# Kernel optimization log

Hardware: AMD Instinct MI355X
Metric: run time of the kernel (lower is better)

The kernel has to match this reference:

```python
import jax, jax.numpy as jnp
import numpy as np

SIZE = 512
N_STROKES = 8
N_SAMPLES = 32
STROKE_WIDTH = 0.04


def setup_inputs() -> dict:
    key = jax.random.key(0)
    k1, _ = jax.random.split(key)
    # control points seeded like torch.rand(...) * 0.6 + 0.2
    control_points = jax.random.uniform(k1, (N_STROKES, 4, 2), dtype=jnp.float32) * 0.6 + 0.2
    # pixel grid buffer: (x, y) coords in [0,1], row-major over (y, x)
    coords = jnp.linspace(0.0, 1.0, SIZE, dtype=jnp.float32)
    grid_y, grid_x = jnp.meshgrid(coords, coords, indexing="ij")
    pixel_grid = jnp.stack([grid_x, grid_y], axis=-1).reshape(-1, 2)  # (HW, 2)
    return {"control_points": control_points, "pixel_grid": pixel_grid}


def _bezier3_samples(curves, n_samples):
    # curves: (S, 4, 2) -> (S, n_samples, 2)
    ts = jnp.linspace(0.0, 1.0, n_samples, dtype=curves.dtype)
    t = ts[None, :, None]
    mt = 1.0 - t
    p0, p1, p2, p3 = (curves[:, k:k + 1, :] for k in range(4))
    return mt ** 3 * p0 + 3.0 * mt ** 2 * t * p1 + 3.0 * mt * t ** 2 * p2 + t ** 3 * p3


def reference(control_points, pixel_grid):
    # all_strokes(): symmetric=False, empty stroke_groups -> just clamp
    pts = jnp.clip(control_points, 0.0, 1.0)
    samples = _bezier3_samples(pts, N_SAMPLES).reshape(-1, 2)  # (P, 2), P = S*n_samples
    sharpness = float(N_SAMPLES) * 8.0
    # pairwise distances (HW, P) — soft-min via logsumexp over curve points
    diff = pixel_grid[:, None, :] - samples[None, :, :]          # (HW, P, 2)
    dist = jnp.sqrt(jnp.sum(diff * diff, axis=-1))               # (HW, P)
    min_dist = -jax.nn.logsumexp(-sharpness * dist, axis=-1) / sharpness  # (HW,)
    coverage = jax.nn.sigmoid((STROKE_WIDTH - min_dist) * (8.0 / STROKE_WIDTH))
    return (1.0 - coverage.reshape(SIZE, SIZE))[None]  # (1, H, W)
```

## Files before the change

kernel.cpp:

```cpp
#include <hip/hip_runtime.h>


#define SIZE 512
#define RADIUS 0.06f
#define FARCUT 0.1217f
#define HB 0.01467710f
#define HD 0.02075670f

__device__ __forceinline__ float clamp01(float x) {
    return fminf(fmaxf(x, 0.0f), 1.0f);
}
__device__ __forceinline__ float wave_min(float v) {
    #pragma unroll
    for (int m = 1; m < 64; m <<= 1) v = fminf(v, __shfl_xor(v, m));
    return v;
}
__device__ __forceinline__ float wave_max(float v) {
    #pragma unroll
    for (int m = 1; m < 64; m <<= 1) v = fmaxf(v, __shfl_xor(v, m));
    return v;
}

__global__ __launch_bounds__(256) void bezier_glyph_kernel(
        const float* __restrict__ cp,
        float* __restrict__ out)
{
    __shared__ float2 list1[260];
    __shared__ float2 list2[260];
    __shared__ float  redbuf[8];
    __shared__ int    n1s, n2s;

    const int tid  = threadIdx.x;
    const int lane = tid & 63;
    const int wid  = tid >> 6;
    if (tid == 0) { n1s = 0; n2s = 0; }

    const int b        = blockIdx.x;
    const int row_base = (b >> 5) << 4;
    const int col_base = (b & 31) << 4;
    const float inv = 1.0f / 511.0f;
    const float cx  = ((float)col_base + 7.5f) * inv;
    const float cy  = ((float)row_base + 7.5f) * inv;

    float sx, sy, dc, bb2;
    {
        const int s = tid >> 5, j = tid & 31;
        const float* p = cp + s * 8;
        const float x0 = clamp01(p[0]), y0 = clamp01(p[1]);
        const float x1 = clamp01(p[2]), y1 = clamp01(p[3]);
        const float x2 = clamp01(p[4]), y2 = clamp01(p[5]);
        const float x3 = clamp01(p[6]), y3 = clamp01(p[7]);
        const float u  = (float)j * (1.0f / 31.0f);
        const float mu = 1.0f - u;
        const float w0 = mu * mu * mu;
        const float w1 = 3.0f * mu * mu * u;
        const float w2 = 3.0f * mu * u * u;
        const float w3 = u * u * u;
        sx = w0 * x0 + w1 * x1 + w2 * x2 + w3 * x3;
        sy = w0 * y0 + w1 * y1 + w2 * y2 + w3 * y3;
        const float dcx = sx - cx, dcy = sy - cy;
        dc = __builtin_amdgcn_sqrtf(dcx * dcx + dcy * dcy);
        const float bx = fmaxf(fabsf(dcx) - HB, 0.0f);
        const float by = fmaxf(fabsf(dcy) - HB, 0.0f);
        bb2 = bx * bx + by * by;
    }

    {
        const float wm = wave_min(dc);
        if (lane == 0) redbuf[wid] = wm;
    }
    __syncthreads();
    const float Dc = fminf(fminf(redbuf[0], redbuf[1]),
                           fminf(redbuf[2], redbuf[3]));
    const float T1 = fminf(Dc, FARCUT + HD) + 2.0f * HD + 1e-4f;

    {
        const bool keep = (dc <= T1);
        const unsigned long long mk = __ballot(keep);
        int base = 0;
        if (lane == 0) base = atomicAdd(&n1s, (int)__popcll(mk));
        base = __shfl(base, 0);
        if (keep) {
            const int pos = base + (int)__popcll(mk & ((1ull << lane) - 1ull));
            list1[pos] = make_float2(sx, sy);
        }
    }
    __syncthreads();
    const int n1 = n1s;
    if (tid < 4) list1[n1 + tid] = make_float2(1e3f, 1e3f);
    __syncthreads();

    const int row = row_base + (tid >> 4);
    const int col = col_base + (tid & 15);
    const float py = (float)row * inv;
    const float px = (float)col * inv;

    float m = 3e38f;
    const int n1r = (n1 + 3) & ~3;
    for (int k = 0; k < n1r; k += 4) {
        const float2 a = list1[k],     b2 = list1[k + 1];
        const float2 c = list1[k + 2], e  = list1[k + 3];
        float dx, dy;
        dx = px - a.x;  dy = py - a.y;  const float qa = fmaf(dx, dx, dy * dy);
        dx = px - b2.x; dy = py - b2.y; const float qb = fmaf(dx, dx, dy * dy);
        dx = px - c.x;  dy = py - c.y;  const float qc = fmaf(dx, dx, dy * dy);
        dx = px - e.x;  dy = py - e.y;  const float qe = fmaf(dx, dx, dy * dy);
        m = fminf(m, fminf(fminf(qa, qb), fminf(qc, qe)));
    }
    const float d   = __builtin_amdgcn_sqrtf(m);
    const float cap = fminf(d, FARCUT);

    {
        const float wdm = wave_min(d);
        const float wcm = wave_max(cap);
        if (lane == 0) { redbuf[wid] = wdm; redbuf[4 + wid] = wcm; }
    }
    __syncthreads();
    const float dminblk = fminf(fminf(redbuf[0], redbuf[1]),
                                fminf(redbuf[2], redbuf[3]));
    const float Tmax    = fmaxf(fmaxf(redbuf[4], redbuf[5]),
                                fmaxf(redbuf[6], redbuf[7]));

    if (dminblk > FARCUT) {
        out[row * SIZE + col] = 1.0f;
        return;
    }

    {
        const float T2 = Tmax + RADIUS + 1e-4f;
        const bool keep = (bb2 <= T2 * T2);
        const unsigned long long mk = __ballot(keep);
        int base = 0;
        if (lane == 0) base = atomicAdd(&n2s, (int)__popcll(mk));
        base = __shfl(base, 0);
        if (keep) {
            const int pos = base + (int)__popcll(mk & ((1ull << lane) - 1ull));
            list2[pos] = make_float2(sx, sy);
        }
    }
    __syncthreads();
    const int n2 = n2s;
    if (tid < 4) list2[n2 + tid] = make_float2(1e3f, 1e3f);
    __syncthreads();

    const float C  = 369.3299304675766f;
    const float nC = -C;
    const float cd = C * d;
    float S = 0.0f;
    const int n2r = (n2 + 3) & ~3;
    for (int k = 0; k < n2r; k += 4) {
        const float2 a = list2[k],     b2 = list2[k + 1];
        const float2 c = list2[k + 2], e  = list2[k + 3];
        float dx, dy;
        dx = px - a.x;  dy = py - a.y;  const float qa = fmaf(dx, dx, dy * dy);
        dx = px - b2.x; dy = py - b2.y; const float qb = fmaf(dx, dx, dy * dy);
        dx = px - c.x;  dy = py - c.y;  const float qc = fmaf(dx, dx, dy * dy);
        dx = px - e.x;  dy = py - e.y;  const float qe = fmaf(dx, dx, dy * dy);
        S += __builtin_amdgcn_exp2f(fmaf(nC, __builtin_amdgcn_sqrtf(qa), cd))
           + __builtin_amdgcn_exp2f(fmaf(nC, __builtin_amdgcn_sqrtf(qb), cd))
           + __builtin_amdgcn_exp2f(fmaf(nC, __builtin_amdgcn_sqrtf(qc), cd))
           + __builtin_amdgcn_exp2f(fmaf(nC, __builtin_amdgcn_sqrtf(qe), cd));
    }

    const float md = d - __builtin_amdgcn_logf(S) * (1.0f / C);
    const float K  = 288.53900817779268f;
    const float o  = __builtin_amdgcn_rcpf(
                        1.0f + __builtin_amdgcn_exp2f((0.04f - md) * K));
    out[row * SIZE + col] = o;
}

extern "C" void kernel_launch(void* const* d_in, const int* in_sizes, int n_in,
                              void* d_out, int out_size, void* d_ws, size_t ws_size,
                              hipStream_t stream) {
    const float* cp = (const float*)d_in[0];
    float* out = (float*)d_out;
    bezier_glyph_kernel<<<dim3(1024), dim3(256), 0, stream>>>(cp, out);
}
```

Before: 60.50 us.

## Shrink pixel tiles to 8x8 single-wave blocks with wave-level culling

Each block now covers an 8x8 pixel tile in a single 64-lane wave instead of a 16x16 tile across four waves. Every lane builds four curve samples, and the candidate lists are compacted with ballot/popcount only, with no shared counters, atomics or cross-wave reductions. The cull bounds (HB, HD) shrink to match the smaller tile, so each tile keeps fewer candidate samples and more tiles can exit early. In exchange there are four times as many blocks, and every block repeats the curve sampling work.

Result: no change. 59.37 us (-1.9%).

```diff
diff --git a/kernel.cpp b/kernel.cpp
--- a/kernel.cpp
+++ b/kernel.cpp
@@ -4,8 +4,8 @@
 #define SIZE 512
 #define RADIUS 0.06f
 #define FARCUT 0.1217f
-#define HB 0.01467710f
-#define HD 0.02075670f
+#define HB 0.00684932f
+#define HD 0.00968631f
 
 __device__ __forceinline__ float clamp01(float x) {
     return fminf(fmaxf(x, 0.0f), 1.0f);
@@ -21,77 +21,76 @@
     return v;
 }
 
-__global__ __launch_bounds__(256) void bezier_glyph_kernel(
+__global__ __launch_bounds__(64) void bezier_glyph_kernel(
         const float* __restrict__ cp,
         float* __restrict__ out)
 {
     __shared__ float2 list1[260];
     __shared__ float2 list2[260];
-    __shared__ float  redbuf[8];
-    __shared__ int    n1s, n2s;
 
-    const int tid  = threadIdx.x;
-    const int lane = tid & 63;
-    const int wid  = tid >> 6;
-    if (tid == 0) { n1s = 0; n2s = 0; }
+    const int tid = threadIdx.x;
+    const int b   = blockIdx.x;
+    const int row_base = (b >> 6) << 3;
+    const int col_base = (b & 63) << 3;
+    const float inv = 1.0f / 511.0f;
+    const float cx  = ((float)col_base + 3.5f) * inv;
+    const float cy  = ((float)row_base + 3.5f) * inv;
 
-    const int b        = blockIdx.x;
-    const int row_base = (b >> 5) << 4;
-    const int col_base = (b & 31) << 4;
-    const float inv = 1.0f / 511.0f;
-    const float cx  = ((float)col_base + 7.5f) * inv;
-    const float cy  = ((float)row_base + 7.5f) * inv;
-
-    float sx, sy, dc, bb2;
+    float sxv[4], syv[4], dc2v[4], bb2v[4];
     {
-        const int s = tid >> 5, j = tid & 31;
+        const int s = tid >> 3;
         const float* p = cp + s * 8;
         const float x0 = clamp01(p[0]), y0 = clamp01(p[1]);
         const float x1 = clamp01(p[2]), y1 = clamp01(p[3]);
         const float x2 = clamp01(p[4]), y2 = clamp01(p[5]);
         const float x3 = clamp01(p[6]), y3 = clamp01(p[7]);
-        const float u  = (float)j * (1.0f / 31.0f);
-        const float mu = 1.0f - u;
-        const float w0 = mu * mu * mu;
-        const float w1 = 3.0f * mu * mu * u;
-        const float w2 = 3.0f * mu * u * u;
-        const float w3 = u * u * u;
-        sx = w0 * x0 + w1 * x1 + w2 * x2 + w3 * x3;
-        sy = w0 * y0 + w1 * y1 + w2 * y2 + w3 * y3;
-        const float dcx = sx - cx, dcy = sy - cy;
-        dc = __builtin_amdgcn_sqrtf(dcx * dcx + dcy * dcy);
-        const float bx = fmaxf(fabsf(dcx) - HB, 0.0f);
-        const float by = fmaxf(fabsf(dcy) - HB, 0.0f);
-        bb2 = bx * bx + by * by;
+        #pragma unroll
+        for (int r = 0; r < 4; ++r) {
+            const int j    = ((tid << 2) + r) & 31;
+            const float u  = (float)j * (1.0f / 31.0f);
+            const float mu = 1.0f - u;
+            const float w0 = mu * mu * mu;
+            const float w1 = 3.0f * mu * mu * u;
+            const float w2 = 3.0f * mu * u * u;
+            const float w3 = u * u * u;
+            const float sx = w0 * x0 + w1 * x1 + w2 * x2 + w3 * x3;
+            const float sy = w0 * y0 + w1 * y1 + w2 * y2 + w3 * y3;
+            sxv[r] = sx; syv[r] = sy;
+            const float dcx = sx - cx, dcy = sy - cy;
+            dc2v[r] = dcx * dcx + dcy * dcy;
+            const float bx = fmaxf(fabsf(dcx) - HB, 0.0f);
+            const float by = fmaxf(fabsf(dcy) - HB, 0.0f);
+            bb2v[r] = bx * bx + by * by;
+        }
     }
 
-    {
-        const float wm = wave_min(dc);
-        if (lane == 0) redbuf[wid] = wm;
+    const float Dc = __builtin_amdgcn_sqrtf(wave_min(
+        fminf(fminf(dc2v[0], dc2v[1]), fminf(dc2v[2], dc2v[3]))));
+    const float T1  = fminf(Dc, FARCUT + HD) + 2.0f * HD + 1e-4f;
+    const float T1s = T1 * T1;
+
+    const unsigned long long lt = (tid == 63) ? ~0ull >> 1
+                                              : (1ull << tid) - 1ull;
+    int n1 = 0;
+    #pragma unroll
+    for (int r = 0; r < 4; ++r) {
+        const bool keep = (dc2v[r] <= T1s);
+        const unsigned long long mk = __ballot(keep);
+        if (keep)
+            list1[n1 + (int)__popcll(mk & lt)] = make_float2(sxv[r], syv[r]);
+        n1 += (int)__popcll(mk);
     }
-    __syncthreads();
-    const float Dc = fminf(fminf(redbuf[0], redbuf[1]),
-                           fminf(redbuf[2], redbuf[3]));
-    const float T1 = fminf(Dc, FARCUT + HD) + 2.0f * HD + 1e-4f;
 
-    {
-        const bool keep = (dc <= T1);
-        const unsigned long long mk = __ballot(keep);
-        int base = 0;
-        if (lane == 0) base = atomicAdd(&n1s, (int)__popcll(mk));
-        base = __shfl(base, 0);
-        if (keep) {
-            const int pos = base + (int)__popcll(mk & ((1ull << lane) - 1ull));
-            list1[pos] = make_float2(sx, sy);
-        }
+    const int row = row_base + (tid >> 3);
+    const int col = col_base + (tid & 7);
+
+    if (n1 == 0) {
+        out[row * SIZE + col] = 1.0f;
+        return;
     }
-    __syncthreads();
-    const int n1 = n1s;
     if (tid < 4) list1[n1 + tid] = make_float2(1e3f, 1e3f);
     __syncthreads();
 
-    const int row = row_base + (tid >> 4);
-    const int col = col_base + (tid & 15);
     const float py = (float)row * inv;
     const float px = (float)col * inv;
 
@@ -110,36 +109,25 @@
     const float d   = __builtin_amdgcn_sqrtf(m);
     const float cap = fminf(d, FARCUT);
 
-    {
-        const float wdm = wave_min(d);
-        const float wcm = wave_max(cap);
-        if (lane == 0) { redbuf[wid] = wdm; redbuf[4 + wid] = wcm; }
-    }
-    __syncthreads();
-    const float dminblk = fminf(fminf(redbuf[0], redbuf[1]),
-                                fminf(redbuf[2], redbuf[3]));
-    const float Tmax    = fmaxf(fmaxf(redbuf[4], redbuf[5]),
-                                fmaxf(redbuf[6], redbuf[7]));
+    const float dminw = wave_min(d);
+    const float Tmax  = wave_max(cap);
 
-    if (dminblk > FARCUT) {
+    if (dminw > FARCUT) {
         out[row * SIZE + col] = 1.0f;
         return;
     }
 
-    {
-        const float T2 = Tmax + RADIUS + 1e-4f;
-        const bool keep = (bb2 <= T2 * T2);
+    const float T2  = Tmax + RADIUS + 1e-4f;
+    const float T2s = T2 * T2;
+    int n2 = 0;
+    #pragma unroll
+    for (int r = 0; r < 4; ++r) {
+        const bool keep = (bb2v[r] <= T2s);
         const unsigned long long mk = __ballot(keep);
-        int base = 0;
-        if (lane == 0) base = atomicAdd(&n2s, (int)__popcll(mk));
-        base = __shfl(base, 0);
-        if (keep) {
-            const int pos = base + (int)__popcll(mk & ((1ull << lane) - 1ull));
-            list2[pos] = make_float2(sx, sy);
-        }
+        if (keep)
+            list2[n2 + (int)__popcll(mk & lt)] = make_float2(sxv[r], syv[r]);
+        n2 += (int)__popcll(mk);
     }
-    __syncthreads();
-    const int n2 = n2s;
     if (tid < 4) list2[n2 + tid] = make_float2(1e3f, 1e3f);
     __syncthreads();
 
@@ -164,9 +152,8 @@
 
     const float md = d - __builtin_amdgcn_logf(S) * (1.0f / C);
     const float K  = 288.53900817779268f;
-    const float o  = __builtin_amdgcn_rcpf(
-                        1.0f + __builtin_amdgcn_exp2f((0.04f - md) * K));
-    out[row * SIZE + col] = o;
+    out[row * SIZE + col] = __builtin_amdgcn_rcpf(
+        1.0f + __builtin_amdgcn_exp2f((0.04f - md) * K));
 }
 
 extern "C" void kernel_launch(void* const* d_in, const int* in_sizes, int n_in,
@@ -174,5 +161,5 @@
                               hipStream_t stream) {
     const float* cp = (const float*)d_in[0];
     float* out = (float*)d_out;
-    bezier_glyph_kernel<<<dim3(1024), dim3(256), 0, stream>>>(cp, out);
+    bezier_glyph_kernel<<<dim3(4096), dim3(64), 0, stream>>>(cp, out);
 }
```
